# Optimization experiments

Measured on AMD Instinct MI355X. Metric: run time of the kernel, lower is better.

## Reference

```python
import jax, jax.numpy as jnp
import numpy as np

NUM_HEADS = 16
NUM_KV_HEADS = 4
HEAD_DIM = 128
D_MODEL = 2048


def setup_inputs() -> dict:
    key = jax.random.key(0)
    ks = jax.random.split(key, 6)
    B, S, d = 2, 2048, D_MODEL
    s_in = 1.0 / np.sqrt(d)
    return {
        "inputs_q": jax.random.normal(ks[0], (B, S, d), jnp.float32),
        "wq": jax.random.normal(ks[1], (d, NUM_HEADS * HEAD_DIM), jnp.float32) * s_in,
        "bq": jnp.zeros((NUM_HEADS * HEAD_DIM,), jnp.float32),
        "wk": jax.random.normal(ks[2], (d, NUM_KV_HEADS * HEAD_DIM), jnp.float32) * s_in,
        "bk": jnp.zeros((NUM_KV_HEADS * HEAD_DIM,), jnp.float32),
        "wv": jax.random.normal(ks[3], (d, NUM_KV_HEADS * HEAD_DIM), jnp.float32) * s_in,
        "bv": jnp.zeros((NUM_KV_HEADS * HEAD_DIM,), jnp.float32),
        "wo": jax.random.normal(ks[4], (NUM_HEADS * HEAD_DIM, d), jnp.float32) * s_in,
        "bo": jnp.zeros((d,), jnp.float32),
    }


def reference(inputs_q, wq, bq, wk, bk, wv, bv, wo, bo):
    B, S, _ = inputs_q.shape
    H, Hk, D = NUM_HEADS, NUM_KV_HEADS, HEAD_DIM
    G = H // Hk  # num_key_value_groups
    og_dtype = inputs_q.dtype

    # QKV projections (self-attention: inputs_kv is None)
    xq = (inputs_q @ wq + bq).reshape(B, S, H, D)
    xk = (inputs_q @ wk + bk).reshape(B, S, Hk, D)
    xv = (inputs_q @ wv + bv).reshape(B, S, Hk, D)

    # float32_attention upcast
    xq = xq.astype(jnp.float32)
    xk = xk.astype(jnp.float32)

    # GQA: q grouped as [B,S,Hk,G,D]; equivalent to repeat_interleave of k/v
    scale = 1.0 / np.sqrt(D)
    qg = (xq * scale).reshape(B, S, Hk, G, D)
    # attn_weights: [B, Hk, G, q, k]
    attn = jnp.einsum('bqhgd,bkhd->bhgqk', qg, xk)
    attn = jax.nn.softmax(attn.astype(jnp.float32), axis=-1).astype(xq.dtype)
    # dropout_p = 0.0 -> no-op
    out = jnp.einsum('bhgqk,bkhd->bqhgd', attn.astype(xv.dtype), xv)
    out = out.astype(og_dtype).reshape(B, S, H * D)
    return out @ wo + bo
```

## Files before the change

kernel.cpp:

```cpp
#include <hip/hip_runtime.h>


typedef __attribute__((ext_vector_type(4))) float f32x4;
typedef __attribute__((ext_vector_type(8))) short s16x8;
typedef __attribute__((ext_vector_type(4))) short s16x4;

__device__ __forceinline__ short f2bf(float f) {
  unsigned u = __builtin_bit_cast(unsigned, f);
  u += 0x7fffu + ((u >> 16) & 1u);
  return (short)(u >> 16);
}

__device__ __forceinline__ f32x4 mfma_bf16_16x16x32(s16x8 a, s16x8 b, f32x4 c) {
  asm("v_mfma_f32_16x16x32_bf16 %0, %1, %2, %0" : "+v"(c) : "v"(a), "v"(b));
  return c;
}

__device__ __forceinline__ void gload_lds16(const void* g, void* l) {
  __builtin_amdgcn_global_load_lds(
      (const __attribute__((address_space(1))) unsigned*)g,
      (__attribute__((address_space(3))) unsigned*)l, 16, 0, 0);
}

__global__ void k_cast(const float* __restrict__ in, short* __restrict__ out, int n4) {
  int i = blockIdx.x * blockDim.x + threadIdx.x;
  int stride = gridDim.x * blockDim.x;
  const f32x4* in4 = (const f32x4*)in;
  s16x4* out4 = (s16x4*)out;
  for (; i < n4; i += stride) {
    f32x4 v = in4[i];
    s16x4 o;
    o.x = f2bf(v.x); o.y = f2bf(v.y); o.z = f2bf(v.z); o.w = f2bf(v.w);
    out4[i] = o;
  }
}

__global__ void k_transpose_cast(const float* __restrict__ in, short* __restrict__ out,
                                 int R, int C) {
  __shared__ float t[32][33];
  int tx = threadIdx.x, ty = threadIdx.y;
  int c0 = blockIdx.x * 32, r0 = blockIdx.y * 32;
#pragma unroll
  for (int i = 0; i < 4; ++i)
    t[ty + 8 * i][tx] = in[(size_t)(r0 + ty + 8 * i) * C + (c0 + tx)];
  __syncthreads();
#pragma unroll
  for (int i = 0; i < 4; ++i)
    out[(size_t)(c0 + ty + 8 * i) * R + (r0 + tx)] = f2bf(t[tx][ty + 8 * i]);
}

template <int MODE>
__global__ __launch_bounds__(256) void k_gemm(const short* __restrict__ A,
                                              const short* __restrict__ Bt,
                                              const float* __restrict__ b0,
                                              const float* __restrict__ b1,
                                              const float* __restrict__ b2,
                                              void* __restrict__ Cout,
                                              short* __restrict__ Kc,
                                              short* __restrict__ Vc,
                                              int M, int N, int K) {
  __shared__ __align__(16) short lA[128 * 64];
  __shared__ __align__(16) short lB[128 * 64];
  const int tid = threadIdx.x;
  const int l = tid & 63, w = tid >> 6;
  const int ql = l & 15, g = l >> 4;
  const int wm = w >> 1, wn = w & 1;
  const int m0 = blockIdx.y * 128, n0 = blockIdx.x * 128;
  const int sr = l >> 3, sc = l & 7;

  f32x4 acc[4][4];
#pragma unroll
  for (int ii = 0; ii < 4; ++ii)
#pragma unroll
    for (int jj = 0; jj < 4; ++jj) acc[ii][jj] = (f32x4){0.f, 0.f, 0.f, 0.f};

  const int ktiles = K >> 6;
  for (int kt = 0; kt < ktiles; ++kt) {
    __syncthreads();
#pragma unroll
    for (int i = 0; i < 4; ++i) {
      int r = w * 32 + i * 8 + sr;
      int cg = sc ^ (r & 7);
      gload_lds16(A + (size_t)(m0 + r) * K + kt * 64 + cg * 8,
                  &lA[(w * 32 + i * 8) * 64]);
    }
#pragma unroll
    for (int i = 0; i < 4; ++i) {
      int r = w * 32 + i * 8 + sr;
      int cg = sc ^ (r & 7);
      gload_lds16(Bt + (size_t)(n0 + r) * K + kt * 64 + cg * 8,
                  &lB[(w * 32 + i * 8) * 64]);
    }
    __syncthreads();
#pragma unroll
    for (int ks = 0; ks < 2; ++ks) {
      s16x8 af[4], bf[4];
#pragma unroll
      for (int mi = 0; mi < 4; ++mi) {
        int r = wm * 64 + mi * 16 + ql;
        int ch = (ks * 4 + g) ^ (r & 7);
        af[mi] = *(const s16x8*)&lA[r * 64 + ch * 8];
      }
#pragma unroll
      for (int ni = 0; ni < 4; ++ni) {
        int r = wn * 64 + ni * 16 + ql;
        int ch = (ks * 4 + g) ^ (r & 7);
        bf[ni] = *(const s16x8*)&lB[r * 64 + ch * 8];
      }
#pragma unroll
      for (int mi = 0; mi < 4; ++mi)
#pragma unroll
        for (int ni = 0; ni < 4; ++ni)
          acc[mi][ni] = mfma_bf16_16x16x32(af[mi], bf[ni], acc[mi][ni]);
    }
  }

#pragma unroll
  for (int mi = 0; mi < 4; ++mi) {
#pragma unroll
    for (int ni = 0; ni < 4; ++ni) {
      int col = n0 + wn * 64 + ni * 16 + ql;
      int row0 = m0 + wm * 64 + mi * 16 + g * 4;
      float bias;
      if (MODE == 0)
        bias = (col < 2048) ? b0[col] : (col < 2560 ? b1[col - 2048] : b2[col - 2560]);
      else
        bias = b0[col];
      f32x4 v = acc[mi][ni];
      if (MODE == 0) {
        if (col < 2048) {
          short* Qb = (short*)Cout;
#pragma unroll
          for (int j = 0; j < 4; ++j)
            Qb[(size_t)(row0 + j) * 2048 + col] = f2bf(v[j] + bias);
        } else if (col < 2560) {
          int c = col - 2048, hk = c >> 7, d = c & 127;
          int ks2 = d >> 5, g2 = (d >> 3) & 3, pos = d & 7;
#pragma unroll
          for (int j = 0; j < 4; ++j) {
            int row = row0 + j, b2 = row >> 11, s = row & 2047;
            int T = s >> 4, lane = (s & 15) + 16 * g2;
            size_t idx = ((((size_t)(b2 * 4 + hk) * 128 + T) * 4 + ks2) * 64 + lane) * 8 + pos;
            Kc[idx] = f2bf(v[j] + bias);
          }
        } else {
          int c = col - 2560, hk = c >> 7, dd = c & 127;
          int dt2 = dd >> 4, ql2 = dd & 15;
#pragma unroll
          for (int j = 0; j < 4; ++j) {
            int row = row0 + j, b2 = row >> 11, s = row & 2047;
            int U = s >> 6, kvs = (s >> 5) & 1, g2 = (s >> 3) & 3, pos = s & 7;
            int lane = ql2 + 16 * g2;
            size_t idx = (((((size_t)(b2 * 4 + hk) * 32 + U) * 2 + kvs) * 8 + dt2) * 64 + lane) * 8 + pos;
            Vc[idx] = f2bf(v[j] + bias);
          }
        }
      } else {
        float* C = (float*)Cout;
#pragma unroll
        for (int j = 0; j < 4; ++j) C[(size_t)(row0 + j) * N + col] = v[j] + bias;
      }
    }
  }
}

__global__ __launch_bounds__(512, 4) void k_attn(const short* __restrict__ Qb,
                                                 const short* __restrict__ Kc,
                                                 const short* __restrict__ Vc,
                                                 short* __restrict__ Out) {
  __shared__ __align__(16) char smem[16384 + 16384 + 8 * 2304];
  short* lK = (short*)smem;
  short* lV = (short*)(smem + 16384);
  const int tid = threadIdx.x;
  const int l = tid & 63, w = tid >> 6;
  const int ql = l & 15, g = l >> 4;

  const int LID = blockIdx.x;
  const int grp = LID & 7;
  const int j = LID >> 3;
  const int b = grp >> 2, hk = grp & 3;
  const int h = hk * 4 + (j >> 4);
  const int bx = j & 15;
  const int bh = b * 4 + hk;

  const int q0 = bx * 128 + w * 16;
  const short* qp = Qb + (size_t)b * 2048 * 2048 + h * 128;
  const short* kcb = Kc + (size_t)bh * 512 * 512;
  const short* vcb = Vc + (size_t)bh * 512 * 512;
  short(*P)[72] = (short(*)[72])(smem + 32768 + w * 2304);
  short* OLb = (short*)(smem + w * 4608);

  s16x8 qreg[4];
#pragma unroll
  for (int ks = 0; ks < 4; ++ks)
    qreg[ks] = *(const s16x8*)(qp + (size_t)(q0 + ql) * 2048 + ks * 32 + g * 8);

  float mo[4], ls[4];
#pragma unroll
  for (int jj = 0; jj < 4; ++jj) { mo[jj] = -1e30f; ls[jj] = 0.f; }
  f32x4 ot[8];
#pragma unroll
  for (int dt = 0; dt < 8; ++dt) ot[dt] = (f32x4){0.f, 0.f, 0.f, 0.f};

  const float scale = 0.08838834764831845f;

  for (int kt = 0; kt < 32; ++kt) {
    __syncthreads();
#pragma unroll
    for (int i = 0; i < 2; ++i) {
      int s = w * 2 + i;
      gload_lds16(kcb + ((size_t)kt * 16 + s) * 512 + l * 8, (char*)lK + s * 1024);
      gload_lds16(vcb + ((size_t)kt * 16 + s) * 512 + l * 8, (char*)lV + s * 1024);
    }
    __syncthreads();

    s16x8 kf[16];
#pragma unroll
    for (int f = 0; f < 16; ++f)
      kf[f] = *(const s16x8*)(lK + f * 512 + l * 8);

    f32x4 st[4];
#pragma unroll
    for (int t = 0; t < 4; ++t) st[t] = (f32x4){0.f, 0.f, 0.f, 0.f};
#pragma unroll
    for (int t = 0; t < 4; ++t)
#pragma unroll
      for (int ks = 0; ks < 4; ++ks)
        st[t] = mfma_bf16_16x16x32(qreg[ks], kf[t * 4 + ks], st[t]);

    float fac[4];
#pragma unroll
    for (int jj = 0; jj < 4; ++jj) {
#pragma unroll
      for (int t = 0; t < 4; ++t) st[t][jj] *= scale;
      float mt = fmaxf(fmaxf(st[0][jj], st[1][jj]), fmaxf(st[2][jj], st[3][jj]));
      mt = fmaxf(mt, __shfl_xor(mt, 1));
      mt = fmaxf(mt, __shfl_xor(mt, 2));
      mt = fmaxf(mt, __shfl_xor(mt, 4));
      mt = fmaxf(mt, __shfl_xor(mt, 8));
      float mn = fmaxf(mo[jj], mt);
      fac[jj] = __expf(mo[jj] - mn);
      mo[jj] = mn;
#pragma unroll
      for (int t = 0; t < 4; ++t) st[t][jj] = __expf(st[t][jj] - mn);
      float rs = st[0][jj] + st[1][jj] + st[2][jj] + st[3][jj];
      rs += __shfl_xor(rs, 1);
      rs += __shfl_xor(rs, 2);
      rs += __shfl_xor(rs, 4);
      rs += __shfl_xor(rs, 8);
      ls[jj] = ls[jj] * fac[jj] + rs;
    }

#pragma unroll
    for (int t = 0; t < 4; ++t)
#pragma unroll
      for (int jj = 0; jj < 4; ++jj)
        P[g * 4 + jj][t * 16 + ql] = f2bf(st[t][jj]);

    {
      int j2 = ql & 3;
      float fv = (j2 == 0) ? fac[0] : ((j2 == 1) ? fac[1] : ((j2 == 2) ? fac[2] : fac[3]));
      float facq = __shfl(fv, ((ql >> 2) << 4) | ql);
#pragma unroll
      for (int dt = 0; dt < 8; ++dt) {
        ot[dt][0] *= facq; ot[dt][1] *= facq; ot[dt][2] *= facq; ot[dt][3] *= facq;
      }
    }

    s16x8 vf[16];
#pragma unroll
    for (int f = 0; f < 16; ++f)
      vf[f] = *(const s16x8*)(lV + f * 512 + l * 8);
    s16x8 pf0 = *(const s16x8*)&P[ql][0 * 32 + g * 8];
    s16x8 pf1 = *(const s16x8*)&P[ql][1 * 32 + g * 8];
#pragma unroll
    for (int dt = 0; dt < 8; ++dt)
      ot[dt] = mfma_bf16_16x16x32(vf[dt], pf0, ot[dt]);
#pragma unroll
    for (int dt = 0; dt < 8; ++dt)
      ot[dt] = mfma_bf16_16x16x32(vf[8 + dt], pf1, ot[dt]);
  }

  __syncthreads();

  float iv[4];
#pragma unroll
  for (int jj = 0; jj < 4; ++jj) iv[jj] = 1.f / ls[jj];
  int j2 = ql & 3;
  float fv = (j2 == 0) ? iv[0] : ((j2 == 1) ? iv[1] : ((j2 == 2) ? iv[2] : iv[3]));
  float invq = __shfl(fv, ((ql >> 2) << 4) | ql);
#pragma unroll
  for (int dt = 0; dt < 8; ++dt)
#pragma unroll
    for (int jj = 0; jj < 4; ++jj)
      OLb[ql * 136 + dt * 16 + g * 4 + jj] = f2bf(ot[dt][jj] * invq);
#pragma unroll
  for (int pass = 0; pass < 4; ++pass) {
    int r = pass * 4 + g;
    s16x8 o = *(const s16x8*)&OLb[r * 136 + ql * 8];
    *(s16x8*)(Out + (size_t)(b * 2048 + q0 + r) * 2048 + h * 128 + ql * 8) = o;
  }
}

extern "C" void kernel_launch(void* const* d_in, const int* in_sizes, int n_in,
                              void* d_out, int out_size, void* d_ws, size_t ws_size,
                              hipStream_t stream) {
  const float* x  = (const float*)d_in[0];
  const float* wq = (const float*)d_in[1];
  const float* bq = (const float*)d_in[2];
  const float* wk = (const float*)d_in[3];
  const float* bk = (const float*)d_in[4];
  const float* wv = (const float*)d_in[5];
  const float* bv = (const float*)d_in[6];
  const float* wo = (const float*)d_in[7];
  const float* bo = (const float*)d_in[8];
  float* out = (float*)d_out;

  char* ws = (char*)d_ws;
  short* Xb   = (short*)(ws);
  short* Wqkv = (short*)(ws + (size_t)(16u << 20));
  short* WoT  = (short*)(ws + (size_t)(28u << 20));
  short* Qb   = (short*)(ws + (size_t)(36u << 20));
  short* Kc   = (short*)(ws + (size_t)(52u << 20));
  short* Vc   = (short*)(ws + (size_t)(56u << 20));

  dim3 tb(32, 8);

  k_cast<<<2048, 256, 0, stream>>>(x, Xb, 4096 * 2048 / 4);
  k_transpose_cast<<<dim3(64, 64), tb, 0, stream>>>(wq, Wqkv, 2048, 2048);
  k_transpose_cast<<<dim3(16, 64), tb, 0, stream>>>(wk, Wqkv + (size_t)2048 * 2048, 2048, 512);
  k_transpose_cast<<<dim3(16, 64), tb, 0, stream>>>(wv, Wqkv + (size_t)2560 * 2048, 2048, 512);
  k_transpose_cast<<<dim3(64, 64), tb, 0, stream>>>(wo, WoT, 2048, 2048);

  k_gemm<0><<<dim3(3072 / 128, 4096 / 128), 256, 0, stream>>>(
      Xb, Wqkv, bq, bk, bv, (void*)Qb, Kc, Vc, 4096, 3072, 2048);

  k_attn<<<dim3(512), 512, 0, stream>>>(Qb, Kc, Vc, Xb);

  k_gemm<1><<<dim3(2048 / 128, 4096 / 128), 256, 0, stream>>>(
      Xb, WoT, bo, bo, bo, (void*)out, nullptr, nullptr, 4096, 2048, 2048);
}
```

Baseline: 247.4 us.

## Merge weight transpose launches and double-buffer V tile loads in attention

Replaces the four weight transpose-cast launches with one launch that picks the weight matrix from blockIdx.z. Blocks beyond the column range exit early, which cuts per-launch overhead. In the attention kernel, V tiles are double-buffered: the next V tile is prefetched into the alternate LDS buffer while the current one is used, with a partial vmcnt wait. This adds 16KB of LDS per block, which may reduce occupancy under launch_bounds(512,4).

Result: faster. 242.1 us (-2.1%).

```diff
diff --git a/kernel.cpp b/kernel.cpp
--- a/kernel.cpp
+++ b/kernel.cpp
@@ -35,11 +35,25 @@
   }
 }
 
-__global__ void k_transpose_cast(const float* __restrict__ in, short* __restrict__ out,
-                                 int R, int C) {
+__global__ void k_transpose_cast_all(const float* __restrict__ wq,
+                                     const float* __restrict__ wk,
+                                     const float* __restrict__ wv,
+                                     const float* __restrict__ wo,
+                                     short* __restrict__ Wqkv,
+                                     short* __restrict__ WoT) {
   __shared__ float t[32][33];
+  const int which = blockIdx.z;
+  const float* in;
+  short* out;
+  int C;
+  if (which == 0)      { in = wq; out = Wqkv;                          C = 2048; }
+  else if (which == 1) { in = wk; out = Wqkv + (size_t)2048 * 2048;    C = 512;  }
+  else if (which == 2) { in = wv; out = Wqkv + (size_t)2560 * 2048;    C = 512;  }
+  else                 { in = wo; out = WoT;                           C = 2048; }
+  const int R = 2048;
+  int c0 = blockIdx.x * 32, r0 = blockIdx.y * 32;
+  if (c0 >= C) return;
   int tx = threadIdx.x, ty = threadIdx.y;
-  int c0 = blockIdx.x * 32, r0 = blockIdx.y * 32;
 #pragma unroll
   for (int i = 0; i < 4; ++i)
     t[ty + 8 * i][tx] = in[(size_t)(r0 + ty + 8 * i) * C + (c0 + tx)];
@@ -168,9 +182,8 @@
                                                  const short* __restrict__ Kc,
                                                  const short* __restrict__ Vc,
                                                  short* __restrict__ Out) {
-  __shared__ __align__(16) char smem[16384 + 16384 + 8 * 2304];
+  __shared__ __align__(16) char smem[16384 + 32768 + 8 * 2304];
   short* lK = (short*)smem;
-  short* lV = (short*)(smem + 16384);
   const int tid = threadIdx.x;
   const int l = tid & 63, w = tid >> 6;
   const int ql = l & 15, g = l >> 4;
@@ -187,7 +200,7 @@
   const short* qp = Qb + (size_t)b * 2048 * 2048 + h * 128;
   const short* kcb = Kc + (size_t)bh * 512 * 512;
   const short* vcb = Vc + (size_t)bh * 512 * 512;
-  short(*P)[72] = (short(*)[72])(smem + 32768 + w * 2304);
+  short(*P)[72] = (short(*)[72])(smem + 49152 + w * 2304);
   short* OLb = (short*)(smem + w * 4608);
 
   s16x8 qreg[4];
@@ -203,6 +216,12 @@
   for (int dt = 0; dt < 8; ++dt) ot[dt] = (f32x4){0.f, 0.f, 0.f, 0.f};
 
   const float scale = 0.08838834764831845f;
+
+#pragma unroll
+  for (int i = 0; i < 2; ++i) {
+    int s = w * 2 + i;
+    gload_lds16(vcb + (size_t)s * 512 + l * 8, smem + 16384 + s * 1024);
+  }
 
   for (int kt = 0; kt < 32; ++kt) {
     __syncthreads();
@@ -210,9 +229,22 @@
     for (int i = 0; i < 2; ++i) {
       int s = w * 2 + i;
       gload_lds16(kcb + ((size_t)kt * 16 + s) * 512 + l * 8, (char*)lK + s * 1024);
-      gload_lds16(vcb + ((size_t)kt * 16 + s) * 512 + l * 8, (char*)lV + s * 1024);
-    }
-    __syncthreads();
+    }
+    if (kt < 31) {
+#pragma unroll
+      for (int i = 0; i < 2; ++i) {
+        int s = w * 2 + i;
+        gload_lds16(vcb + ((size_t)(kt + 1) * 16 + s) * 512 + l * 8,
+                    smem + 16384 + ((kt + 1) & 1) * 16384 + s * 1024);
+      }
+      asm volatile("s_waitcnt vmcnt(2)" ::: "memory");
+    } else {
+      asm volatile("s_waitcnt vmcnt(0)" ::: "memory");
+    }
+    __builtin_amdgcn_sched_barrier(0);
+    __builtin_amdgcn_s_barrier();
+    __builtin_amdgcn_sched_barrier(0);
+    const short* lV = (const short*)(smem + 16384 + (kt & 1) * 16384);
 
     s16x8 kf[16];
 #pragma unroll
@@ -324,13 +356,9 @@
   short* Kc   = (short*)(ws + (size_t)(52u << 20));
   short* Vc   = (short*)(ws + (size_t)(56u << 20));
 
-  dim3 tb(32, 8);
-
   k_cast<<<2048, 256, 0, stream>>>(x, Xb, 4096 * 2048 / 4);
-  k_transpose_cast<<<dim3(64, 64), tb, 0, stream>>>(wq, Wqkv, 2048, 2048);
-  k_transpose_cast<<<dim3(16, 64), tb, 0, stream>>>(wk, Wqkv + (size_t)2048 * 2048, 2048, 512);
-  k_transpose_cast<<<dim3(16, 64), tb, 0, stream>>>(wv, Wqkv + (size_t)2560 * 2048, 2048, 512);
-  k_transpose_cast<<<dim3(64, 64), tb, 0, stream>>>(wo, WoT, 2048, 2048);
+  k_transpose_cast_all<<<dim3(64, 64, 4), dim3(32, 8), 0, stream>>>(
+      wq, wk, wv, wo, Wqkv, WoT);
 
   k_gemm<0><<<dim3(3072 / 128, 4096 / 128), 256, 0, stream>>>(
       Xb, Wqkv, bq, bk, bv, (void*)Qb, Kc, Vc, 4096, 3072, 2048);
```
